# Kernel optimization log

Hardware: AMD Instinct MI355X
Metric: run time of the kernel (lower is better)

## Reference

```python
import jax, jax.numpy as jnp
import numpy as np


def setup_inputs() -> dict:
    key = jax.random.key(0)
    k1, k2, k3, k4 = jax.random.split(key, 4)
    B, S, D = 4, 2048, 1024
    scale = 1.0 / np.sqrt(D)
    x = jax.random.normal(k1, (B, S, D), dtype=jnp.float32)
    Wq = jax.random.normal(k2, (D, D), dtype=jnp.float32) * scale
    Wk = jax.random.normal(k3, (D, D), dtype=jnp.float32) * scale
    Wv = jax.random.normal(k4, (D, D), dtype=jnp.float32) * scale
    return {"x": x, "Wq": Wq, "Wk": Wk, "Wv": Wv}


def reference(x, Wq, Wk, Wv):
    # x: [B, S, D]; Wq/Wk/Wv: [d_out, d_in] torch Linear convention (y = x @ W.T)
    B, S, D = x.shape
    q = jnp.einsum('bsd,od->bso', x, Wq)
    k = jnp.einsum('bsd,od->bso', x, Wk)
    v = jnp.einsum('bsd,od->bso', x, Wv)
    scores = jnp.einsum('bqo,bko->bqk', q, k)  # [B, S, S]
    causal = jnp.tril(jnp.ones((S, S), dtype=bool))  # True = keep
    scores = jnp.where(causal, scores, -jnp.inf)
    d_out = q.shape[-1]
    attn = jax.nn.softmax(scores / jnp.sqrt(jnp.asarray(d_out, x.dtype)), axis=-1)
    # dropout_prob = 0.0 -> identity
    return jnp.einsum('bqk,bko->bqo', attn, v)
```

## Files before the change

kernel.cpp:

```cpp
#include <hip/hip_runtime.h>
#include <hip/hip_bf16.h>
#include <stdint.h>

typedef __attribute__((ext_vector_type(8))) short bf16x8;
typedef __attribute__((ext_vector_type(4))) float f32x4;

__device__ __forceinline__ float bf2f(unsigned short u) {
    union { unsigned int i; float f; } z; z.i = ((unsigned int)u) << 16; return z.f;
}
__device__ __forceinline__ unsigned short f2bf(float f) {
    union { float f; unsigned int i; } z; z.f = f;
    unsigned int x = z.i;
    unsigned int r = x + 0x7fffu + ((x >> 16) & 1u);
    return (unsigned short)(r >> 16);
}

typedef const __attribute__((address_space(1))) unsigned int* gp_t;
typedef __attribute__((address_space(3))) unsigned int* lp_t;

__device__ __forceinline__ void gload_lds16(const void* g, void* l) {
    __builtin_amdgcn_global_load_lds((gp_t)g, (lp_t)l, 16, 0, 0);
}

__device__ __forceinline__ int xcd_remap(int orig, int nwg) {
    const int q = nwg >> 3, r = nwg & 7;
    const int xcd = orig & 7, pos = orig >> 3;
    return (xcd < r ? xcd * (q + 1) : r * (q + 1) + (xcd - r) * q) + pos;
}

__global__ __launch_bounds__(256) void cvt_x(const float* __restrict__ in,
                                             unsigned short* __restrict__ out, int n4) {
    int i = blockIdx.x * 256 + threadIdx.x;
    int stride = gridDim.x * 256;
    for (; i < n4; i += stride) {
        float4 v = reinterpret_cast<const float4*>(in)[i];
        ushort4 u;
        u.x = f2bf(v.x); u.y = f2bf(v.y); u.z = f2bf(v.z); u.w = f2bf(v.w);
        reinterpret_cast<ushort4*>(out)[i] = u;
    }
}

__global__ __launch_bounds__(256) void cvt_w(const float* __restrict__ wq,
                                             const float* __restrict__ wk,
                                             const float* __restrict__ wv,
                                             unsigned short* __restrict__ out, int n4) {
    const int z = blockIdx.z;
    const float* in = (z == 0) ? wq : (z == 1) ? wk : wv;
    const float scale = (z == 0) ? 0.03125f : 1.0f;
    unsigned short* o = out + (size_t)z * n4 * 4;
    int i = blockIdx.x * 256 + threadIdx.x;
    int stride = gridDim.x * 256;
    for (; i < n4; i += stride) {
        float4 v = reinterpret_cast<const float4*>(in)[i];
        ushort4 u;
        u.x = f2bf(v.x * scale); u.y = f2bf(v.y * scale);
        u.z = f2bf(v.z * scale); u.w = f2bf(v.w * scale);
        reinterpret_cast<ushort4*>(o)[i] = u;
    }
}

#define MFMA(a, b, c) __builtin_amdgcn_mfma_f32_16x16x32_bf16(a, b, c, 0, 0, 0)
#define SB() __builtin_amdgcn_sched_barrier(0)
#define BAR() __builtin_amdgcn_s_barrier()
#define LGKM0() asm volatile("s_waitcnt lgkmcnt(0)" ::: "memory")

__device__ __forceinline__ void gemm256_core(
    const unsigned short* __restrict__ Ab,
    const unsigned short* __restrict__ Bb,
    int m0, int n0,
    unsigned short (&As)[2][256 * 64], unsigned short (&Bs)[2][256 * 64],
    f32x4 (&acc)[8][4])
{
    constexpr int LD = 1024, NK = 16;
    const int tid = threadIdx.x;
    const int l = tid & 63, w = tid >> 6;
    const int wr = w >> 2, wc = w & 3;

    const int srow = w * 8 + (l >> 3);
    const int scol = ((l & 7) ^ (l >> 3)) * 8;
    const size_t ldst = (size_t)w * 1024 + (size_t)l * 16;

    auto stageA = [&](int t, int h, int b) {
        const unsigned short* src = Ab + (size_t)(m0 + h * 128 + srow) * LD + t * 64 + scol;
        char* dst = (char*)&As[b][0] + h * 16384 + ldst;
        gload_lds16(src, dst);
        gload_lds16(src + (size_t)64 * LD, dst + 8192);
    };
    auto stageB = [&](int t, int h, int b) {
        const unsigned short* src = Bb + (size_t)(n0 + h * 128 + srow) * LD + t * 64 + scol;
        char* dst = (char*)&Bs[b][0] + h * 16384 + ldst;
        gload_lds16(src, dst);
        gload_lds16(src + (size_t)64 * LD, dst + 8192);
    };

    const int l15 = l & 15, l7 = l & 7;
    const int s0 = (((l >> 4) ^ l7) * 16);
    const int s1 = ((((l >> 4) + 4) ^ l7) * 16);

    bf16x8 Af[4][2], Bf0[2][2], Bf1[2][2];

    stageA(0, 0, 0); stageA(0, 1, 0); stageB(0, 0, 0); stageB(0, 1, 0);
    stageB(1, 0, 1); stageB(1, 1, 1);
    asm volatile("s_waitcnt vmcnt(4)" ::: "memory");
    SB(); BAR(); SB();

    for (int t = 0; t < NK; ++t) {
        const int b = t & 1, bn = b ^ 1;
        const char* ab = (const char*)&As[b][0] + (wr * 128 + l15) * 128;
        const char* bb = (const char*)&Bs[b][0] + (wc * 64 + l15) * 128;

        #pragma unroll
        for (int mi = 0; mi < 4; ++mi) {
            Af[mi][0] = *(const bf16x8*)(ab + mi * 2048 + s0);
            Af[mi][1] = *(const bf16x8*)(ab + mi * 2048 + s1);
        }
        #pragma unroll
        for (int ni = 0; ni < 2; ++ni) {
            Bf0[ni][0] = *(const bf16x8*)(bb + ni * 2048 + s0);
            Bf0[ni][1] = *(const bf16x8*)(bb + ni * 2048 + s1);
        }
        if (t + 1 < NK) stageA(t + 1, 0, bn);
        BAR(); LGKM0(); SB();
        __builtin_amdgcn_s_setprio(1);
        #pragma unroll
        for (int mi = 0; mi < 4; ++mi)
            #pragma unroll
            for (int ni = 0; ni < 2; ++ni) {
                acc[mi][ni] = MFMA(Af[mi][0], Bf0[ni][0], acc[mi][ni]);
                acc[mi][ni] = MFMA(Af[mi][1], Bf0[ni][1], acc[mi][ni]);
            }
        __builtin_amdgcn_s_setprio(0);
        SB(); BAR(); SB();

        #pragma unroll
        for (int ni = 0; ni < 2; ++ni) {
            Bf1[ni][0] = *(const bf16x8*)(bb + 4096 + ni * 2048 + s0);
            Bf1[ni][1] = *(const bf16x8*)(bb + 4096 + ni * 2048 + s1);
        }
        if (t + 1 < NK) stageA(t + 1, 1, bn);
        BAR(); LGKM0(); SB();
        __builtin_amdgcn_s_setprio(1);
        #pragma unroll
        for (int mi = 0; mi < 4; ++mi)
            #pragma unroll
            for (int ni = 0; ni < 2; ++ni) {
                acc[mi][2 + ni] = MFMA(Af[mi][0], Bf1[ni][0], acc[mi][2 + ni]);
                acc[mi][2 + ni] = MFMA(Af[mi][1], Bf1[ni][1], acc[mi][2 + ni]);
            }
        __builtin_amdgcn_s_setprio(0);
        SB(); BAR(); SB();

        #pragma unroll
        for (int mi = 0; mi < 4; ++mi) {
            Af[mi][0] = *(const bf16x8*)(ab + 8192 + mi * 2048 + s0);
            Af[mi][1] = *(const bf16x8*)(ab + 8192 + mi * 2048 + s1);
        }
        if (t + 2 < NK) stageB(t + 2, 0, b);
        BAR(); LGKM0(); SB();
        __builtin_amdgcn_s_setprio(1);
        #pragma unroll
        for (int mi = 0; mi < 4; ++mi)
            #pragma unroll
            for (int ni = 0; ni < 2; ++ni) {
                acc[4 + mi][2 + ni] = MFMA(Af[mi][0], Bf1[ni][0], acc[4 + mi][2 + ni]);
                acc[4 + mi][2 + ni] = MFMA(Af[mi][1], Bf1[ni][1], acc[4 + mi][2 + ni]);
            }
        __builtin_amdgcn_s_setprio(0);
        SB(); BAR(); SB();

        if (t + 2 < NK) stageB(t + 2, 1, b);
        BAR(); SB();
        __builtin_amdgcn_s_setprio(1);
        #pragma unroll
        for (int mi = 0; mi < 4; ++mi)
            #pragma unroll
            for (int ni = 0; ni < 2; ++ni) {
                acc[4 + mi][ni] = MFMA(Af[mi][0], Bf0[ni][0], acc[4 + mi][ni]);
                acc[4 + mi][ni] = MFMA(Af[mi][1], Bf0[ni][1], acc[4 + mi][ni]);
            }
        __builtin_amdgcn_s_setprio(0);
        if (t + 2 < NK) {
            asm volatile("s_waitcnt vmcnt(4)" ::: "memory");
        } else if (t + 1 < NK) {
            asm volatile("s_waitcnt vmcnt(0)" ::: "memory");
        }
        SB(); BAR(); SB();
    }
}

__global__ __launch_bounds__(512, 2) void qk_proj(
    const unsigned short* __restrict__ xb, const unsigned short* __restrict__ wqkv,
    unsigned short* __restrict__ qb, unsigned short* __restrict__ kb)
{
    const int wg = xcd_remap(blockIdx.x, 256);
    const int mt = wg & 31, nt = wg >> 5;
    const int m0 = mt * 256, n0 = nt * 256;

    __shared__ unsigned short As[2][256 * 64];
    __shared__ unsigned short Bs[2][256 * 64];
    f32x4 acc[8][4] = {};

    gemm256_core(xb, wqkv, m0, n0, As, Bs, acc);

    const int tid = threadIdx.x;
    const int l = tid & 63, w = tid >> 6;
    const int wr = w >> 2, wc = w & 3;
    const int crow = (l >> 4) * 4, ccol = l & 15;
    unsigned short* C = (nt < 4) ? qb : kb;
    const int cb = (nt < 4) ? n0 : n0 - 1024;
    #pragma unroll
    for (int mi = 0; mi < 8; ++mi)
        #pragma unroll
        for (int ni = 0; ni < 4; ++ni) {
            const size_t rbase = (size_t)(m0 + wr * 128 + mi * 16 + crow);
            const size_t cg = (size_t)(cb + wc * 64 + ni * 16 + ccol);
            #pragma unroll
            for (int r = 0; r < 4; ++r)
                C[(rbase + r) * 1024 + cg] = f2bf(acc[mi][ni][r]);
        }
}

__device__ __forceinline__ void gemm128_core64(
    const unsigned short* __restrict__ Ab, int lda,
    const unsigned short* __restrict__ Bb, int ldb,
    int m0, int n0, int nk,
    unsigned short (&As)[2][128 * 64], unsigned short (&Bs)[2][128 * 64],
    f32x4 (&acc)[4][4])
{
    const int tid = threadIdx.x;
    const int l = tid & 63, w = tid >> 6;
    const int wr = w >> 1, wc = w & 1;
    const int l15 = l & 15;

    const int srow = w * 8 + (l >> 3);
    const int scol = ((l & 7) ^ (l >> 3)) * 8;
    const size_t ldst = (size_t)w * 1024 + (size_t)l * 16;

    auto stage = [&](int t, int b) {
        const int k0 = t * 64;
        #pragma unroll
        for (int i = 0; i < 4; ++i) {
            gload_lds16(Ab + (size_t)(m0 + i * 32 + srow) * lda + k0 + scol,
                        (char*)&As[b][0] + i * 4096 + ldst);
            gload_lds16(Bb + (size_t)(n0 + i * 32 + srow) * ldb + k0 + scol,
                        (char*)&Bs[b][0] + i * 4096 + ldst);
        }
    };

    const int s0 = (((l >> 4) ^ (l & 7)) * 16);
    const int s1 = ((((l >> 4) + 4) ^ (l & 7)) * 16);

    stage(0, 0);
    if (nk > 1) {
        stage(1, 1);
        asm volatile("s_waitcnt vmcnt(8)" ::: "memory");
    } else {
        asm volatile("s_waitcnt vmcnt(0)" ::: "memory");
    }
    SB(); BAR(); SB();

    for (int t = 0; t < nk; ++t) {
        const int b = t & 1;
        const char* ab = (const char*)&As[b][0] + (wr * 64 + l15) * 128;
        const char* bb = (const char*)&Bs[b][0] + (wc * 64 + l15) * 128;
        bf16x8 af[4][2], bfr[4][2];
        #pragma unroll
        for (int m = 0; m < 4; ++m) {
            af[m][0] = *(const bf16x8*)(ab + m * 2048 + s0);
            af[m][1] = *(const bf16x8*)(ab + m * 2048 + s1);
        }
        #pragma unroll
        for (int n = 0; n < 4; ++n) {
            bfr[n][0] = *(const bf16x8*)(bb + n * 2048 + s0);
            bfr[n][1] = *(const bf16x8*)(bb + n * 2048 + s1);
        }
        LGKM0(); SB();
        BAR(); SB();
        if (t + 2 < nk) stage(t + 2, b);

        __builtin_amdgcn_s_setprio(1);
        #pragma unroll
        for (int m = 0; m < 4; ++m)
            #pragma unroll
            for (int n = 0; n < 4; ++n) {
                acc[m][n] = MFMA(af[m][0], bfr[n][0], acc[m][n]);
                acc[m][n] = MFMA(af[m][1], bfr[n][1], acc[m][n]);
            }
        __builtin_amdgcn_s_setprio(0);

        if (t + 2 < nk) {
            asm volatile("s_waitcnt vmcnt(8)" ::: "memory");
        } else if (t + 1 < nk) {
            asm volatile("s_waitcnt vmcnt(0)" ::: "memory");
        }
        SB(); BAR(); SB();
    }
}

__global__ __launch_bounds__(256) void v_scores128(
    const unsigned short* __restrict__ xb, const unsigned short* __restrict__ wv,
    const unsigned short* __restrict__ qb, const unsigned short* __restrict__ kb,
    unsigned short* __restrict__ vt, unsigned short* __restrict__ sc)
{
    const int wg = xcd_remap(blockIdx.x, 1056);

    __shared__ unsigned short As[2][128 * 64];
    __shared__ unsigned short Bs[2][128 * 64];
    f32x4 acc[4][4] = {};

    const int tid = threadIdx.x;
    const int l = tid & 63, w = tid >> 6;
    const int wr = w >> 1, wc = w & 1;
    const int crow = (l >> 4) * 4, ccol = l & 15;

    if (wg < 512) {
        const int mt = wg & 63, nt = wg >> 6;
        const int m0 = mt * 128, n0 = nt * 128;
        gemm128_core64(xb, 1024, wv, 1024, m0, n0, 16, As, Bs, acc);
        #pragma unroll
        for (int m = 0; m < 4; ++m)
            #pragma unroll
            for (int n = 0; n < 4; ++n) {
                const int rbase = m0 + wr * 64 + m * 16 + crow;
                const int o = n0 + wc * 64 + n * 16 + ccol;
                ushort4 u;
                u.x = f2bf(acc[m][n][0]);
                u.y = f2bf(acc[m][n][1]);
                u.z = f2bf(acc[m][n][2]);
                u.w = f2bf(acc[m][n][3]);
                *reinterpret_cast<ushort4*>(&vt[(size_t)o * 8192 + rbase]) = u;
            }
    } else {
        const int s = wg - 512;
        const int z = s / 136, r = s % 136;
        int mt = (int)((__builtin_sqrtf(8.f * r + 1.f) - 1.f) * 0.5f);
        while ((mt + 1) * (mt + 2) / 2 <= r) ++mt;
        while (mt * (mt + 1) / 2 > r) --mt;
        const int nt = r - mt * (mt + 1) / 2;
        const int m0 = mt * 128, n0 = nt * 128;
        const unsigned short* Ab = qb + (size_t)z * 2048 * 1024;
        const unsigned short* Bb = kb + (size_t)z * 2048 * 1024;
        gemm128_core64(Ab, 1024, Bb, 1024, m0, n0, 16, As, Bs, acc);
        unsigned short* C = sc + (size_t)z * 2048 * 2048;
        #pragma unroll
        for (int m = 0; m < 4; ++m)
            #pragma unroll
            for (int n = 0; n < 4; ++n) {
                const size_t rbase = (size_t)(m0 + wr * 64 + m * 16 + crow);
                const size_t cg = (size_t)(n0 + wc * 64 + n * 16 + ccol);
                #pragma unroll
                for (int r2 = 0; r2 < 4; ++r2)
                    C[(rbase + r2) * 2048 + cg] = f2bf(acc[m][n][r2]);
            }
    }
}

__global__ __launch_bounds__(256) void gemm128_pv(
    const unsigned short* __restrict__ A, int lda, long long sA,
    const unsigned short* __restrict__ B, int ldb, long long sB,
    float* __restrict__ C, int ldc, long long sC, int K)
{
    const int GX = gridDim.x, GY = gridDim.y;
    const int nwg = GX * GY * gridDim.z;
    const int orig = blockIdx.x + GX * (blockIdx.y + GY * blockIdx.z);
    const int wgid = xcd_remap(orig, nwg);
    const int mt = wgid % GX;
    const int tq = wgid / GX;
    const int nt = tq % GY, z = tq / GY;

    const unsigned short* Ab = A + (size_t)z * sA;
    const unsigned short* Bb = B + (size_t)z * sB;
    const int Keff = ((mt + 1) * 128 < K) ? (mt + 1) * 128 : K;
    const int nk = Keff >> 6;

    __shared__ unsigned short As[2][128 * 64];
    __shared__ unsigned short Bs[2][128 * 64];
    f32x4 acc[4][4] = {};

    gemm128_core64(Ab, lda, Bb, ldb, mt * 128, nt * 128, nk, As, Bs, acc);

    const int tid = threadIdx.x;
    const int l = tid & 63, w = tid >> 6;
    const int wr = w >> 1, wc = w & 1;
    const int crow = (l >> 4) * 4, ccol = l & 15;
    float* Cb = C + (size_t)z * sC;
    #pragma unroll
    for (int m = 0; m < 4; ++m)
        #pragma unroll
        for (int n = 0; n < 4; ++n) {
            const size_t rbase = (size_t)(mt * 128 + wr * 64 + m * 16 + crow);
            const size_t cg = (size_t)(nt * 128 + wc * 64 + n * 16 + ccol);
            #pragma unroll
            for (int r = 0; r < 4; ++r)
                Cb[(rbase + r) * ldc + cg] = acc[m][n][r];
        }
}

__global__ __launch_bounds__(256) void softmax_causal(unsigned short* __restrict__ P) {
    const int S = 2048;
    const int gq = blockIdx.x;
    const int q = gq & (S - 1);
    unsigned short* row = P + (size_t)gq * S;
    const int t = threadIdx.x;
    const int c0 = t * 8;
    const int l = t & 63, w = t >> 6;
    const int wlim = ((q >> 7) + 1) << 7;
    const float NEG = -__builtin_huge_valf();

    float f[8];
    if (c0 <= q) {
        uint4 rv = *reinterpret_cast<const uint4*>(row + c0);
        unsigned short us[8];
        us[0] = rv.x & 0xffff; us[1] = rv.x >> 16;
        us[2] = rv.y & 0xffff; us[3] = rv.y >> 16;
        us[4] = rv.z & 0xffff; us[5] = rv.z >> 16;
        us[6] = rv.w & 0xffff; us[7] = rv.w >> 16;
        #pragma unroll
        for (int i = 0; i < 8; ++i)
            f[i] = (c0 + i <= q) ? bf2f(us[i]) : NEG;
    } else {
        #pragma unroll
        for (int i = 0; i < 8; ++i) f[i] = NEG;
    }

    float m = f[0];
    #pragma unroll
    for (int i = 1; i < 8; ++i) m = fmaxf(m, f[i]);
    #pragma unroll
    for (int o = 1; o < 64; o <<= 1) m = fmaxf(m, __shfl_xor(m, o));

    __shared__ float smax[4], ssum[4];
    if (l == 0) smax[w] = m;
    __syncthreads();
    m = fmaxf(fmaxf(smax[0], smax[1]), fmaxf(smax[2], smax[3]));

    float e[8];
    float s = 0.f;
    #pragma unroll
    for (int i = 0; i < 8; ++i) {
        e[i] = exp2f((f[i] - m) * 1.44269504f);
        s += e[i];
    }
    #pragma unroll
    for (int o = 1; o < 64; o <<= 1) s += __shfl_xor(s, o);
    if (l == 0) ssum[w] = s;
    __syncthreads();
    s = ssum[0] + ssum[1] + ssum[2] + ssum[3];
    const float inv = 1.0f / s;

    if (c0 < wlim) {
        uint4 ov;
        ov.x = f2bf(e[0] * inv) | ((unsigned int)f2bf(e[1] * inv) << 16);
        ov.y = f2bf(e[2] * inv) | ((unsigned int)f2bf(e[3] * inv) << 16);
        ov.z = f2bf(e[4] * inv) | ((unsigned int)f2bf(e[5] * inv) << 16);
        ov.w = f2bf(e[6] * inv) | ((unsigned int)f2bf(e[7] * inv) << 16);
        *reinterpret_cast<uint4*>(row + c0) = ov;
    }
}

extern "C" void kernel_launch(void* const* d_in, const int* in_sizes, int n_in,
                              void* d_out, int out_size, void* d_ws, size_t ws_size,
                              hipStream_t stream) {
    const float* x  = (const float*)d_in[0];
    const float* Wq = (const float*)d_in[1];
    const float* Wk = (const float*)d_in[2];
    const float* Wv = (const float*)d_in[3];
    float* out = (float*)d_out;

    const int Bz = 4, S = 2048, D = 1024;
    const int MS = Bz * S;
    const int DD = D * D;

    char* ws = (char*)d_ws;
    unsigned short* xb   = (unsigned short*)(ws);
    unsigned short* wqkv = (unsigned short*)(ws + (16ull << 20));
    unsigned short* qb   = (unsigned short*)(ws + (22ull << 20));
    unsigned short* kb   = (unsigned short*)(ws + (38ull << 20));
    unsigned short* vt   = (unsigned short*)(ws + (54ull << 20));
    unsigned short* sc   = (unsigned short*)(ws + (70ull << 20));

    cvt_x<<<2048, 256, 0, stream>>>(x, xb, MS * D / 4);
    cvt_w<<<dim3(512, 1, 3), 256, 0, stream>>>(Wq, Wk, Wv, wqkv, DD / 4);

    qk_proj<<<256, 512, 0, stream>>>(xb, wqkv, qb, kb);

    v_scores128<<<1056, 256, 0, stream>>>(xb, wqkv + (size_t)2 * DD, qb, kb, vt, sc);

    softmax_causal<<<MS, 256, 0, stream>>>(sc);

    gemm128_pv<<<dim3(S / 128, D / 128, Bz), 256, 0, stream>>>(
        sc, S, (long long)S * S, vt, MS, S, out, D, (long long)S * D, S);
}
```

Before: 159.9 us.

## Merge conversion kernels, one-wave-per-row softmax, causal-balanced PV tile ordering

Merges the x and weight bf16 conversion kernels into one launch, saving a kernel launch. Softmax now gives each wavefront one full row, so the cross-wave LDS reductions and __syncthreads are gone. The PV GEMM grid is flattened and remapped so that the first 256 blocks take the short causal tiles and the second half takes the long ones in mirrored order, to balance work across XCDs. The risk is that per-thread register use in softmax goes up, and the new tile ordering may hurt L2 locality.

```diff
diff --git a/kernel.cpp b/kernel.cpp
--- a/kernel.cpp
+++ b/kernel.cpp
@@ -28,34 +28,37 @@
     return (xcd < r ? xcd * (q + 1) : r * (q + 1) + (xcd - r) * q) + pos;
 }
 
-__global__ __launch_bounds__(256) void cvt_x(const float* __restrict__ in,
-                                             unsigned short* __restrict__ out, int n4) {
+__global__ __launch_bounds__(256) void cvt_all(
+    const float* __restrict__ x, const float* __restrict__ wq,
+    const float* __restrict__ wk, const float* __restrict__ wv,
+    unsigned short* __restrict__ xb, unsigned short* __restrict__ wqkv) {
+    const int NX = 1 << 21;
+    const int DD4 = 1 << 18;
+    const int total = NX + 3 * DD4;
     int i = blockIdx.x * 256 + threadIdx.x;
-    int stride = gridDim.x * 256;
-    for (; i < n4; i += stride) {
-        float4 v = reinterpret_cast<const float4*>(in)[i];
-        ushort4 u;
-        u.x = f2bf(v.x); u.y = f2bf(v.y); u.z = f2bf(v.z); u.w = f2bf(v.w);
-        reinterpret_cast<ushort4*>(out)[i] = u;
-    }
-}
-
-__global__ __launch_bounds__(256) void cvt_w(const float* __restrict__ wq,
-                                             const float* __restrict__ wk,
-                                             const float* __restrict__ wv,
-                                             unsigned short* __restrict__ out, int n4) {
-    const int z = blockIdx.z;
-    const float* in = (z == 0) ? wq : (z == 1) ? wk : wv;
-    const float scale = (z == 0) ? 0.03125f : 1.0f;
-    unsigned short* o = out + (size_t)z * n4 * 4;
-    int i = blockIdx.x * 256 + threadIdx.x;
-    int stride = gridDim.x * 256;
-    for (; i < n4; i += stride) {
-        float4 v = reinterpret_cast<const float4*>(in)[i];
+    const int stride = gridDim.x * 256;
+    for (; i < total; i += stride) {
+        const float* src;
+        ushort4* dst;
+        float scale = 1.0f;
+        int idx;
+        if (i < NX) {
+            src = x; dst = (ushort4*)xb; idx = i;
+        } else {
+            const int j = i - NX;
+            const int r = j >> 18;
+            src = (r == 0) ? wq : (r == 1) ? wk : wv;
+            if (r == 0) scale = 0.03125f;
+            dst = (ushort4*)wqkv + (size_t)r * DD4;
+            idx = j & (DD4 - 1);
+            dst -= (size_t)0;
+            dst += 0;
+        }
+        float4 v = reinterpret_cast<const float4*>(src)[idx];
         ushort4 u;
         u.x = f2bf(v.x * scale); u.y = f2bf(v.y * scale);
         u.z = f2bf(v.z * scale); u.w = f2bf(v.w * scale);
-        reinterpret_cast<ushort4*>(o)[i] = u;
+        dst[idx] = u;
     }
 }
 
@@ -360,13 +363,14 @@
     const unsigned short* __restrict__ B, int ldb, long long sB,
     float* __restrict__ C, int ldc, long long sC, int K)
 {
-    const int GX = gridDim.x, GY = gridDim.y;
-    const int nwg = GX * GY * gridDim.z;
-    const int orig = blockIdx.x + GX * (blockIdx.y + GY * blockIdx.z);
-    const int wgid = xcd_remap(orig, nwg);
-    const int mt = wgid % GX;
-    const int tq = wgid / GX;
-    const int nt = tq % GY, z = tq / GY;
+    const int orig = blockIdx.x;
+    const int h = orig >> 8;
+    const int c = xcd_remap(orig & 255, 256);
+    const int z = c >> 6;
+    const int rem = c & 63;
+    const int nt = rem >> 3;
+    const int j = rem & 7;
+    const int mt = h ? (15 - j) : j;
 
     const unsigned short* Ab = A + (size_t)z * sA;
     const unsigned short* Bb = B + (size_t)z * sB;
@@ -398,63 +402,64 @@
 
 __global__ __launch_bounds__(256) void softmax_causal(unsigned short* __restrict__ P) {
     const int S = 2048;
-    const int gq = blockIdx.x;
+    const int w = threadIdx.x >> 6, l = threadIdx.x & 63;
+    const int gq = blockIdx.x * 4 + w;
     const int q = gq & (S - 1);
     unsigned short* row = P + (size_t)gq * S;
-    const int t = threadIdx.x;
-    const int c0 = t * 8;
-    const int l = t & 63, w = t >> 6;
     const int wlim = ((q >> 7) + 1) << 7;
     const float NEG = -__builtin_huge_valf();
 
-    float f[8];
-    if (c0 <= q) {
-        uint4 rv = *reinterpret_cast<const uint4*>(row + c0);
-        unsigned short us[8];
-        us[0] = rv.x & 0xffff; us[1] = rv.x >> 16;
-        us[2] = rv.y & 0xffff; us[3] = rv.y >> 16;
-        us[4] = rv.z & 0xffff; us[5] = rv.z >> 16;
-        us[6] = rv.w & 0xffff; us[7] = rv.w >> 16;
-        #pragma unroll
-        for (int i = 0; i < 8; ++i)
-            f[i] = (c0 + i <= q) ? bf2f(us[i]) : NEG;
-    } else {
-        #pragma unroll
-        for (int i = 0; i < 8; ++i) f[i] = NEG;
-    }
-
-    float m = f[0];
-    #pragma unroll
-    for (int i = 1; i < 8; ++i) m = fmaxf(m, f[i]);
+    float f[4][8];
+    #pragma unroll
+    for (int p = 0; p < 4; ++p) {
+        const int c0 = p * 512 + l * 8;
+        if (p * 512 <= q && c0 <= q) {
+            uint4 rv = *reinterpret_cast<const uint4*>(row + c0);
+            unsigned short us[8];
+            us[0] = rv.x & 0xffff; us[1] = rv.x >> 16;
+            us[2] = rv.y & 0xffff; us[3] = rv.y >> 16;
+            us[4] = rv.z & 0xffff; us[5] = rv.z >> 16;
+            us[6] = rv.w & 0xffff; us[7] = rv.w >> 16;
+            #pragma unroll
+            for (int i = 0; i < 8; ++i)
+                f[p][i] = (c0 + i <= q) ? bf2f(us[i]) : NEG;
+        } else {
+            #pragma unroll
+            for (int i = 0; i < 8; ++i) f[p][i] = NEG;
+        }
+    }
+
+    float m = NEG;
+    #pragma unroll
+    for (int p = 0; p < 4; ++p)
+        #pragma unroll
+        for (int i = 0; i < 8; ++i) m = fmaxf(m, f[p][i]);
     #pragma unroll
     for (int o = 1; o < 64; o <<= 1) m = fmaxf(m, __shfl_xor(m, o));
 
-    __shared__ float smax[4], ssum[4];
-    if (l == 0) smax[w] = m;
-    __syncthreads();
-    m = fmaxf(fmaxf(smax[0], smax[1]), fmaxf(smax[2], smax[3]));
-
-    float e[8];
     float s = 0.f;
     #pragma unroll
-    for (int i = 0; i < 8; ++i) {
-        e[i] = exp2f((f[i] - m) * 1.44269504f);
-        s += e[i];
-    }
+    for (int p = 0; p < 4; ++p)
+        #pragma unroll
+        for (int i = 0; i < 8; ++i) {
+            f[p][i] = exp2f((f[p][i] - m) * 1.44269504f);
+            s += f[p][i];
+        }
     #pragma unroll
     for (int o = 1; o < 64; o <<= 1) s += __shfl_xor(s, o);
-    if (l == 0) ssum[w] = s;
-    __syncthreads();
-    s = ssum[0] + ssum[1] + ssum[2] + ssum[3];
     const float inv = 1.0f / s;
 
-    if (c0 < wlim) {
-        uint4 ov;
-        ov.x = f2bf(e[0] * inv) | ((unsigned int)f2bf(e[1] * inv) << 16);
-        ov.y = f2bf(e[2] * inv) | ((unsigned int)f2bf(e[3] * inv) << 16);
-        ov.z = f2bf(e[4] * inv) | ((unsigned int)f2bf(e[5] * inv) << 16);
-        ov.w = f2bf(e[6] * inv) | ((unsigned int)f2bf(e[7] * inv) << 16);
-        *reinterpret_cast<uint4*>(row + c0) = ov;
+    #pragma unroll
+    for (int p = 0; p < 4; ++p) {
+        const int c0 = p * 512 + l * 8;
+        if (p * 512 < wlim && c0 < wlim) {
+            uint4 ov;
+            ov.x = f2bf(f[p][0] * inv) | ((unsigned int)f2bf(f[p][1] * inv) << 16);
+            ov.y = f2bf(f[p][2] * inv) | ((unsigned int)f2bf(f[p][3] * inv) << 16);
+            ov.z = f2bf(f[p][4] * inv) | ((unsigned int)f2bf(f[p][5] * inv) << 16);
+            ov.w = f2bf(f[p][6] * inv) | ((unsigned int)f2bf(f[p][7] * inv) << 16);
+            *reinterpret_cast<uint4*>(row + c0) = ov;
+        }
     }
 }
 
@@ -479,15 +484,14 @@
     unsigned short* vt   = (unsigned short*)(ws + (54ull << 20));
     unsigned short* sc   = (unsigned short*)(ws + (70ull << 20));
 
-    cvt_x<<<2048, 256, 0, stream>>>(x, xb, MS * D / 4);
-    cvt_w<<<dim3(512, 1, 3), 256, 0, stream>>>(Wq, Wk, Wv, wqkv, DD / 4);
+    cvt_all<<<2048, 256, 0, stream>>>(x, Wq, Wk, Wv, xb, wqkv);
 
     qk_proj<<<256, 512, 0, stream>>>(xb, wqkv, qb, kb);
 
     v_scores128<<<1056, 256, 0, stream>>>(xb, wqkv + (size_t)2 * DD, qb, kb, vt, sc);
 
-    softmax_causal<<<MS, 256, 0, stream>>>(sc);
-
-    gemm128_pv<<<dim3(S / 128, D / 128, Bz), 256, 0, stream>>>(
+    softmax_causal<<<2048, 256, 0, stream>>>(sc);
+
+    gemm128_pv<<<512, 256, 0, stream>>>(
         sc, S, (long long)S * S, vt, MS, S, out, D, (long long)S * D, S);
 }
```

Measured after the change: 156.8 us. Within noise of the previous version (-2.0%).
